# Kernel optimization log

Measured on AMD Instinct MI355X. Metric: run time of the kernel, lower is better.

Reference implementation:

```python
import jax, jax.numpy as jnp
import numpy as np

B, S, D, H, L, O = 64, 512, 512, 1024, 2, 1000


def setup_inputs() -> dict:
    key = jax.random.key(0)
    ks = jax.random.split(key, 12)
    s = 0.05
    return {
        "x": jax.random.normal(ks[0], (B, S, D), jnp.float32),
        "h0": jnp.zeros((L, B, H), jnp.float32),
        "c0": jnp.zeros((L, B, H), jnp.float32),
        "W_ih0": jax.random.normal(ks[1], (4 * H, D), jnp.float32) * s,
        "W_hh0": jax.random.normal(ks[2], (4 * H, H), jnp.float32) * s,
        "b_ih0": jax.random.normal(ks[3], (4 * H,), jnp.float32) * s,
        "b_hh0": jax.random.normal(ks[4], (4 * H,), jnp.float32) * s,
        "W_ih1": jax.random.normal(ks[5], (4 * H, H), jnp.float32) * s,
        "W_hh1": jax.random.normal(ks[6], (4 * H, H), jnp.float32) * s,
        "b_ih1": jax.random.normal(ks[7], (4 * H,), jnp.float32) * s,
        "b_hh1": jax.random.normal(ks[8], (4 * H,), jnp.float32) * s,
        "W_fc": jax.random.normal(ks[9], (O, H), jnp.float32) * s,
        "b_fc": jax.random.normal(ks[10], (O,), jnp.float32) * s,
    }


def _lstm_cell(x_t, h, c, W_ih, W_hh, b_ih, b_hh):
    # standard LSTMCell: fused 4-gate GEMM, gate order (i, f, g, o)
    gates = x_t @ W_ih.T + b_ih + h @ W_hh.T + b_hh  # [B, 4H]
    i, f, g, o = jnp.split(gates, 4, axis=-1)
    i = jax.nn.sigmoid(i)
    f = jax.nn.sigmoid(f)
    g = jnp.tanh(g)
    o = jax.nn.sigmoid(o)
    c_new = f * c + i * g
    h_new = o * jnp.tanh(c_new)
    return h_new, c_new


def reference(x, h0, c0, W_ih0, W_hh0, b_ih0, b_hh0, W_ih1, W_hh1, b_ih1, b_hh1, W_fc, b_fc):
    params = [(W_ih0, W_hh0, b_ih0, b_hh0), (W_ih1, W_hh1, b_ih1, b_hh1)]

    def step(carry, x_t):
        hs, cs = carry  # tuples of [B,H] per layer
        new_h, new_c = [], []
        inp = x_t
        for l in range(L):  # fixed small layer count
            h_l, c_l = _lstm_cell(inp, hs[l], cs[l], *params[l])
            new_h.append(h_l)
            new_c.append(c_l)
            inp = h_l
        return (tuple(new_h), tuple(new_c)), None

    xs = jnp.swapaxes(x, 0, 1)  # [S, B, D]
    init = (tuple(h0[l] for l in range(L)), tuple(c0[l] for l in range(L)))
    (hs, _), _ = jax.lax.scan(step, init, xs)
    # dropout is inference-mode identity; output_activation=None
    out = hs[-1] @ W_fc.T + b_fc  # [B, O]
    return out
```

## Files before the change

### kernel.cpp

```cpp
#include <hip/hip_runtime.h>

#define B_ 64
#define S_ 512
#define D_ 512
#define H_ 1024

typedef __attribute__((ext_vector_type(8))) short bf16x8;
typedef __attribute__((ext_vector_type(4))) float f32x4;
typedef unsigned short u16;
typedef unsigned int u32;

#define MFMA(a, b, c) __builtin_amdgcn_mfma_f32_16x16x32_bf16(a, b, c, 0, 0, 0)

__device__ __forceinline__ u16 f2bf(float f) {
    u32 u = __float_as_uint(f);
    u += 0x7fffu + ((u >> 16) & 1u);
    return (u16)(u >> 16);
}
__device__ __forceinline__ float sigm(float x) { return 1.0f / (1.0f + __expf(-x)); }
__device__ __forceinline__ float tanh_f(float x) { return 1.0f - 2.0f / (__expf(2.0f * x) + 1.0f); }

__device__ __forceinline__ bf16x8 cvt8(const float* p) {
    float4 f0 = ((const float4*)p)[0];
    float4 f1 = ((const float4*)p)[1];
    bf16x8 v;
    v[0] = (short)f2bf(f0.x); v[1] = (short)f2bf(f0.y);
    v[2] = (short)f2bf(f0.z); v[3] = (short)f2bf(f0.w);
    v[4] = (short)f2bf(f1.x); v[5] = (short)f2bf(f1.y);
    v[6] = (short)f2bf(f1.z); v[7] = (short)f2bf(f1.w);
    return v;
}

__device__ __forceinline__ void llc_ld(bf16x8& d, const u16* p) {
    asm volatile("global_load_dwordx4 %0, %1, off sc0 sc1" : "=v"(d) : "v"(p));
}
__device__ __forceinline__ void vm0() {
    asm volatile("s_waitcnt vmcnt(0)" ::: "memory");
}
__device__ __forceinline__ void fence_frag(bf16x8& d) {
    asm volatile("" : "+v"(d));
}
__device__ __forceinline__ void llc_st16(u16* p, u16 v) {
    u32 vv = v;
    asm volatile("global_store_short %0, %1, off sc0 sc1" :: "v"(p), "v"(vv) : "memory");
}

__global__ void prep_w(const float* __restrict__ Wih, const float* __restrict__ Whh,
                       u16* __restrict__ Wc, int Kx, int Kw, int total8) {
    int idx = blockIdx.x * 256 + threadIdx.x;
    if (idx >= total8) return;
    int kc8 = Kw >> 3;
    int n = idx / kc8;
    int kc = (idx - n * kc8) << 3;
    const float* src = (kc < Kx) ? (Wih + (size_t)n * Kx + kc)
                                 : (Whh + (size_t)n * (Kw - Kx) + (kc - Kx));
    *(bf16x8*)(Wc + (size_t)n * Kw + kc) = cvt8(src);
}

__global__ void prep_misc2(const float* __restrict__ h0in,
                           const float* __restrict__ bih0, const float* __restrict__ bhh0,
                           const float* __restrict__ bih1, const float* __restrict__ bhh1,
                           float* __restrict__ bias0, float* __restrict__ bias1,
                           u16* __restrict__ h0a, u16* __restrict__ h0b,
                           u16* __restrict__ h1a, u16* __restrict__ h1b,
                           int* __restrict__ bar) {
    int idx = blockIdx.x * 256 + threadIdx.x;
    if (idx < 1024) bar[idx] = 0;
    if (idx < 4096) { bias0[idx] = bih0[idx] + bhh0[idx]; return; }
    if (idx < 8192) { int i = idx - 4096; bias1[i] = bih1[i] + bhh1[i]; return; }
    int r = idx - 8192;
    if (r >= 2 * B_ * H_) return;
    int l = r >> 16;
    int rr = r & 65535;
    int b = rr >> 10, col = rr & 1023;
    int sidx = (col >> 3) * 512 + b * 8 + (col & 7);
    u16 hb = f2bf(h0in[r]);
    if (l == 0) { h0a[sidx] = hb; h0b[sidx] = hb; }
    else        { h1a[sidx] = hb; h1b[sidx] = hb; }
}

__global__ __launch_bounds__(512, 2) void lstm_persist(
    const float* __restrict__ x,
    const u16* __restrict__ W0c, const u16* __restrict__ W1c,
    const float* __restrict__ bias0, const float* __restrict__ bias1,
    const float* __restrict__ c0in,
    u16* __restrict__ h0a, u16* __restrict__ h0b,
    u16* __restrict__ h1a, u16* __restrict__ h1b,
    float* __restrict__ h1f,
    int* __restrict__ bar) {
    const int bk = blockIdx.x;
    const int cgp = bk >> 1;
    const int mh = bk & 1;
    const int tid = threadIdx.x;
    const int w = tid >> 6;
    const int lane = tid & 63;
    const int quad = lane >> 4;
    const int l16 = lane & 15;

    int gc[2];
    #pragma unroll
    for (int n = 0; n < 2; ++n) {
        int c = n * 16 + l16;
        gc[n] = (c >> 3) * 1024 + cgp * 8 + (c & 7);
    }

    bf16x8 w0x[2][2], w0h[2][4];
    bf16x8 w1f[2][8];
    #pragma unroll
    for (int n = 0; n < 2; ++n) {
        #pragma unroll
        for (int kf = 0; kf < 2; ++kf)
            w0x[n][kf] = *(const bf16x8*)(W0c + (size_t)gc[n] * 1536 + w * 64 + kf * 32 + quad * 8);
        #pragma unroll
        for (int kf = 0; kf < 4; ++kf)
            w0h[n][kf] = *(const bf16x8*)(W0c + (size_t)gc[n] * 1536 + 512 + w * 128 + kf * 32 + quad * 8);
        #pragma unroll
        for (int kf = 0; kf < 8; ++kf)
            w1f[n][kf] = *(const bf16x8*)(W1c + (size_t)gc[n] * 2048 + w * 256 + kf * 32 + quad * 8);
    }

    __shared__ float part[8 * 32 * 37];
    __shared__ float c0l[256], c1l[256];
    __shared__ float b0l[32], b1l[32];

    if (tid < 32) {
        int gg = tid >> 3, j = tid & 7;
        b0l[tid] = bias0[gg * 1024 + cgp * 8 + j];
        b1l[tid] = bias1[gg * 1024 + cgp * 8 + j];
    }
    if (tid < 256) {
        int b = tid >> 3, j = tid & 7;
        int gi = (mh * 32 + b) * 1024 + cgp * 8 + j;
        c0l[tid] = c0in[gi];
        c1l[tid] = c0in[65536 + gi];
    }
    __syncthreads();

    const int brow0 = mh * 32 + l16;
    const int brow1 = brow0 + 16;

    f32x4 xacc[2][2];
    #define XPART(t)                                                                 \
        {                                                                            \
            xacc[0][0] = (f32x4){0.f,0.f,0.f,0.f}; xacc[0][1] = (f32x4){0.f,0.f,0.f,0.f}; \
            xacc[1][0] = (f32x4){0.f,0.f,0.f,0.f}; xacc[1][1] = (f32x4){0.f,0.f,0.f,0.f}; \
            _Pragma("unroll")                                                        \
            for (int kf = 0; kf < 2; ++kf) {                                         \
                int k = w * 64 + kf * 32 + quad * 8;                                 \
                bf16x8 a0_ = cvt8(x + (size_t)brow0 * 262144 + (t) * 512 + k);       \
                bf16x8 a1_ = cvt8(x + (size_t)brow1 * 262144 + (t) * 512 + k);       \
                xacc[0][0] = MFMA(a0_, w0x[0][kf], xacc[0][0]);                      \
                xacc[0][1] = MFMA(a0_, w0x[1][kf], xacc[0][1]);                      \
                xacc[1][0] = MFMA(a1_, w0x[0][kf], xacc[1][0]);                      \
                xacc[1][1] = MFMA(a1_, w0x[1][kf], xacc[1][1]);                      \
            }                                                                        \
        }

    XPART(0);

    for (int p = 0; p <= S_; ++p) {
        const int rd = p & 1;
        const u16* h0r = rd ? h0b : h0a;
        u16*       h0w_ = rd ? h0a : h0b;
        const u16* h1r = rd ? h1b : h1a;
        u16*       h1w_ = rd ? h1a : h1b;

        if (p > 0) {
            if (tid == 0) {
                int tgt = 256 * p;
                for (int it = 0; it < 20000; ++it) {
                    if (__hip_atomic_load(&bar[0], __ATOMIC_RELAXED, __HIP_MEMORY_SCOPE_AGENT) >= tgt)
                        break;
                    __builtin_amdgcn_s_sleep(1);
                }
            }
            __syncthreads();
        }

        bf16x8 a0[4], a1[4];
        if (p < S_) {
            #pragma unroll
            for (int kf = 0; kf < 4; ++kf) {
                int k8 = w * 16 + kf * 4 + quad;
                llc_ld(a0[kf], h0r + (k8 * 64 + brow0) * 8);
                llc_ld(a1[kf], h0r + (k8 * 64 + brow1) * 8);
            }
            vm0();
            #pragma unroll
            for (int kf = 0; kf < 4; ++kf) { fence_frag(a0[kf]); fence_frag(a1[kf]); }
        }

        if (p < S_) {
            f32x4 acc00 = xacc[0][0], acc01 = xacc[0][1];
            f32x4 acc10 = xacc[1][0], acc11 = xacc[1][1];
            #pragma unroll
            for (int kf = 0; kf < 4; ++kf) {
                acc00 = MFMA(a0[kf], w0h[0][kf], acc00);
                acc01 = MFMA(a0[kf], w0h[1][kf], acc01);
                acc10 = MFMA(a1[kf], w0h[0][kf], acc10);
                acc11 = MFMA(a1[kf], w0h[1][kf], acc11);
            }
            #pragma unroll
            for (int r = 0; r < 4; ++r) {
                int r0 = quad * 4 + r, r1 = 16 + quad * 4 + r;
                part[w * 1184 + r0 * 37 + l16]      = acc00[r];
                part[w * 1184 + r0 * 37 + 16 + l16] = acc01[r];
                part[w * 1184 + r1 * 37 + l16]      = acc10[r];
                part[w * 1184 + r1 * 37 + 16 + l16] = acc11[r];
            }
        }

        if (p >= 1 && tid == 0) {
            int tgt = 256 * p;
            for (int it = 0; it < 20000; ++it) {
                if (__hip_atomic_load(&bar[32], __ATOMIC_RELAXED, __HIP_MEMORY_SCOPE_AGENT) >= tgt)
                    break;
                __builtin_amdgcn_s_sleep(1);
            }
        }
        __syncthreads();

        bf16x8 pb0[8], pb1[8];
        if (p >= 1) {
            #pragma unroll
            for (int kf = 0; kf < 8; ++kf) {
                int k = w * 256 + kf * 32;
                const u16* src = (k < 1024) ? h0r : h1r;
                int k8 = ((k & 1023) >> 3) + quad;
                llc_ld(pb0[kf], src + (k8 * 64 + brow0) * 8);
                llc_ld(pb1[kf], src + (k8 * 64 + brow1) * 8);
            }
        }

        if (p < S_ && tid < 256) {
            int b = tid >> 3, j = tid & 7;
            float g4[4];
            #pragma unroll
            for (int gg = 0; gg < 4; ++gg) {
                float s = b0l[gg * 8 + j];
                #pragma unroll
                for (int w8 = 0; w8 < 8; ++w8)
                    s += part[w8 * 1184 + b * 37 + gg * 8 + j];
                g4[gg] = s;
            }
            float c = c0l[tid];
            float cn = sigm(g4[1]) * c + sigm(g4[0]) * tanh_f(g4[2]);
            float hn = sigm(g4[3]) * tanh_f(cn);
            c0l[tid] = cn;
            llc_st16(h0w_ + cgp * 512 + (mh * 32 + b) * 8 + j, f2bf(hn));
        }
        if (p >= 1) {
            vm0();
            #pragma unroll
            for (int kf = 0; kf < 8; ++kf) { fence_frag(pb0[kf]); fence_frag(pb1[kf]); }
        }
        __syncthreads();
        if (p < S_ && tid == 0)
            __hip_atomic_fetch_add(&bar[0], 1, __ATOMIC_RELAXED, __HIP_MEMORY_SCOPE_AGENT);

        if (p >= 1) {
            f32x4 acc00 = {0.f,0.f,0.f,0.f}, acc01 = {0.f,0.f,0.f,0.f};
            f32x4 acc10 = {0.f,0.f,0.f,0.f}, acc11 = {0.f,0.f,0.f,0.f};
            #pragma unroll
            for (int kf = 0; kf < 8; ++kf) {
                acc00 = MFMA(pb0[kf], w1f[0][kf], acc00);
                acc01 = MFMA(pb0[kf], w1f[1][kf], acc01);
                acc10 = MFMA(pb1[kf], w1f[0][kf], acc10);
                acc11 = MFMA(pb1[kf], w1f[1][kf], acc11);
            }
            #pragma unroll
            for (int r = 0; r < 4; ++r) {
                int r0 = quad * 4 + r, r1 = 16 + quad * 4 + r;
                part[w * 1184 + r0 * 37 + l16]      = acc00[r];
                part[w * 1184 + r0 * 37 + 16 + l16] = acc01[r];
                part[w * 1184 + r1 * 37 + l16]      = acc10[r];
                part[w * 1184 + r1 * 37 + 16 + l16] = acc11[r];
            }
            __syncthreads();
            if (tid < 256) {
                int b = tid >> 3, j = tid & 7;
                float g4[4];
                #pragma unroll
                for (int gg = 0; gg < 4; ++gg) {
                    float s = b1l[gg * 8 + j];
                    #pragma unroll
                    for (int w8 = 0; w8 < 8; ++w8)
                        s += part[w8 * 1184 + b * 37 + gg * 8 + j];
                    g4[gg] = s;
                }
                float c = c1l[tid];
                float cn = sigm(g4[1]) * c + sigm(g4[0]) * tanh_f(g4[2]);
                float hn = sigm(g4[3]) * tanh_f(cn);
                c1l[tid] = cn;
                llc_st16(h1w_ + cgp * 512 + (mh * 32 + b) * 8 + j, f2bf(hn));
                if (p == S_) h1f[(mh * 32 + b) * 1024 + cgp * 8 + j] = hn;
            }
        }

        if (p < S_) {
            __syncthreads();
            if (tid == 0)
                __hip_atomic_fetch_add(&bar[32], 1, __ATOMIC_RELAXED, __HIP_MEMORY_SCOPE_AGENT);
            if (p + 1 < S_) XPART(p + 1);
        }
    }
}

__global__ void fc_k(const float* __restrict__ h1f, const float* __restrict__ Wfc,
                     const float* __restrict__ bfc, float* __restrict__ out) {
    int idx = blockIdx.x * 256 + threadIdx.x;
    if (idx >= 64 * 1000) return;
    int o = idx % 1000;
    int b = idx / 1000;
    const float4* hr = (const float4*)(h1f + b * H_);
    const float4* wr = (const float4*)(Wfc + (size_t)o * H_);
    float s = 0.f;
    #pragma unroll 4
    for (int k = 0; k < 256; ++k) {
        float4 a = hr[k];
        float4 w = wr[k];
        s += a.x * w.x + a.y * w.y + a.z * w.z + a.w * w.w;
    }
    out[idx] = s + bfc[o];
}

extern "C" void kernel_launch(void* const* d_in, const int* in_sizes, int n_in,
                              void* d_out, int out_size, void* d_ws, size_t ws_size,
                              hipStream_t stream) {
    const float* x    = (const float*)d_in[0];
    const float* h0in = (const float*)d_in[1];
    const float* c0in = (const float*)d_in[2];
    const float* Wih0 = (const float*)d_in[3];
    const float* Whh0 = (const float*)d_in[4];
    const float* bih0 = (const float*)d_in[5];
    const float* bhh0 = (const float*)d_in[6];
    const float* Wih1 = (const float*)d_in[7];
    const float* Whh1 = (const float*)d_in[8];
    const float* bih1 = (const float*)d_in[9];
    const float* bhh1 = (const float*)d_in[10];
    const float* Wfc  = (const float*)d_in[11];
    const float* bfc  = (const float*)d_in[12];
    float* out = (float*)d_out;

    char* ws = (char*)d_ws;
    size_t off = 0;
    auto alloc = [&](size_t bytes) {
        void* p = ws + off;
        off += (bytes + 255) & ~(size_t)255;
        return p;
    };
    u16* W0c   = (u16*)alloc((size_t)4096 * 1536 * 2);
    u16* W1c   = (u16*)alloc((size_t)4096 * 2048 * 2);
    float* bias0 = (float*)alloc(4096 * 4);
    float* bias1 = (float*)alloc(4096 * 4);
    u16* h0A   = (u16*)alloc(B_ * H_ * 2);
    u16* h0B   = (u16*)alloc(B_ * H_ * 2);
    u16* h1A   = (u16*)alloc(B_ * H_ * 2);
    u16* h1B   = (u16*)alloc(B_ * H_ * 2);
    float* h1f = (float*)alloc(B_ * H_ * 4);
    int* bar   = (int*)alloc(4096);

    prep_w<<<786432 / 256, 256, 0, stream>>>(Wih0, Whh0, W0c, 512, 1536, 786432);
    prep_w<<<1048576 / 256, 256, 0, stream>>>(Wih1, Whh1, W1c, 1024, 2048, 1048576);
    prep_misc2<<<(8192 + 2 * B_ * H_ + 255) / 256, 256, 0, stream>>>(
        h0in, bih0, bhh0, bih1, bhh1, bias0, bias1, h0A, h0B, h1A, h1B, bar);

    void* args[] = {(void*)&x, (void*)&W0c, (void*)&W1c, (void*)&bias0, (void*)&bias1,
                    (void*)&c0in, (void*)&h0A, (void*)&h0B, (void*)&h1A, (void*)&h1B,
                    (void*)&h1f, (void*)&bar};
    hipLaunchCooperativeKernel((void*)lstm_persist, dim3(256), dim3(512), args, 0, stream);

    fc_k<<<(64000 + 255) / 256, 256, 0, stream>>>(h1f, Wfc, bfc, out);
}
```

Measured before the change: 5.516 ms.

## Triple-buffer layer-0 hidden state and publish it before layer-1 work

Layer 0's hidden state now rotates through three buffers instead of two. Each block finishes the layer-0 cell update and signals the layer-0 barrier before it waits on and computes layer 1, so the next step's layer-0 work can start sooner. The wait at the top of each step now also checks the layer-1 counter from the previous step, which prevents the third buffer from being overwritten while still in use. The next step's x-projection also moves earlier to overlap the layer-1 loads, at the cost of an extra buffer, an extra block-wide sync and a longer spin limit.

```diff
diff --git a/kernel.cpp b/kernel.cpp
--- a/kernel.cpp
+++ b/kernel.cpp
@@ -61,7 +61,7 @@
                            const float* __restrict__ bih0, const float* __restrict__ bhh0,
                            const float* __restrict__ bih1, const float* __restrict__ bhh1,
                            float* __restrict__ bias0, float* __restrict__ bias1,
-                           u16* __restrict__ h0a, u16* __restrict__ h0b,
+                           u16* __restrict__ h0a, u16* __restrict__ h0b, u16* __restrict__ h0c,
                            u16* __restrict__ h1a, u16* __restrict__ h1b,
                            int* __restrict__ bar) {
     int idx = blockIdx.x * 256 + threadIdx.x;
@@ -75,7 +75,7 @@
     int b = rr >> 10, col = rr & 1023;
     int sidx = (col >> 3) * 512 + b * 8 + (col & 7);
     u16 hb = f2bf(h0in[r]);
-    if (l == 0) { h0a[sidx] = hb; h0b[sidx] = hb; }
+    if (l == 0) { h0a[sidx] = hb; h0b[sidx] = hb; h0c[sidx] = hb; }
     else        { h1a[sidx] = hb; h1b[sidx] = hb; }
 }
 
@@ -84,7 +84,7 @@
     const u16* __restrict__ W0c, const u16* __restrict__ W1c,
     const float* __restrict__ bias0, const float* __restrict__ bias1,
     const float* __restrict__ c0in,
-    u16* __restrict__ h0a, u16* __restrict__ h0b,
+    u16* __restrict__ h0a, u16* __restrict__ h0b, u16* __restrict__ h0c,
     u16* __restrict__ h1a, u16* __restrict__ h1b,
     float* __restrict__ h1f,
     int* __restrict__ bar) {
@@ -158,19 +158,23 @@
 
     XPART(0);
 
+    const u16* H0[3] = {h0a, h0b, h0c};
+    int wp = 0;
     for (int p = 0; p <= S_; ++p) {
+        const int rp = (wp == 0) ? 2 : wp - 1;
+        const u16* h0r = H0[rp];
+        u16*       h0w_ = (u16*)H0[wp];
         const int rd = p & 1;
-        const u16* h0r = rd ? h0b : h0a;
-        u16*       h0w_ = rd ? h0a : h0b;
         const u16* h1r = rd ? h1b : h1a;
         u16*       h1w_ = rd ? h1a : h1b;
 
         if (p > 0) {
             if (tid == 0) {
-                int tgt = 256 * p;
-                for (int it = 0; it < 20000; ++it) {
-                    if (__hip_atomic_load(&bar[0], __ATOMIC_RELAXED, __HIP_MEMORY_SCOPE_AGENT) >= tgt)
-                        break;
+                int tgtA = 256 * p, tgtB = 256 * (p - 1);
+                for (int it = 0; it < 40000; ++it) {
+                    int va = __hip_atomic_load(&bar[0], __ATOMIC_RELAXED, __HIP_MEMORY_SCOPE_AGENT);
+                    int vb = __hip_atomic_load(&bar[32], __ATOMIC_RELAXED, __HIP_MEMORY_SCOPE_AGENT);
+                    if (va >= tgtA && vb >= tgtB) break;
                     __builtin_amdgcn_s_sleep(1);
                 }
             }
@@ -188,9 +192,7 @@
             vm0();
             #pragma unroll
             for (int kf = 0; kf < 4; ++kf) { fence_frag(a0[kf]); fence_frag(a1[kf]); }
-        }
-
-        if (p < S_) {
+
             f32x4 acc00 = xacc[0][0], acc01 = xacc[0][1];
             f32x4 acc10 = xacc[1][0], acc11 = xacc[1][1];
             #pragma unroll
@@ -209,10 +211,31 @@
                 part[w * 1184 + r1 * 37 + 16 + l16] = acc11[r];
             }
         }
+        __syncthreads();
+        if (p < S_ && tid < 256) {
+            int b = tid >> 3, j = tid & 7;
+            float g4[4];
+            #pragma unroll
+            for (int gg = 0; gg < 4; ++gg) {
+                float s = b0l[gg * 8 + j];
+                #pragma unroll
+                for (int w8 = 0; w8 < 8; ++w8)
+                    s += part[w8 * 1184 + b * 37 + gg * 8 + j];
+                g4[gg] = s;
+            }
+            float c = c0l[tid];
+            float cn = sigm(g4[1]) * c + sigm(g4[0]) * tanh_f(g4[2]);
+            float hn = sigm(g4[3]) * tanh_f(cn);
+            c0l[tid] = cn;
+            llc_st16(h0w_ + cgp * 512 + (mh * 32 + b) * 8 + j, f2bf(hn));
+        }
+        __syncthreads();
+        if (p < S_ && tid == 0)
+            __hip_atomic_fetch_add(&bar[0], 1, __ATOMIC_RELAXED, __HIP_MEMORY_SCOPE_AGENT);
 
         if (p >= 1 && tid == 0) {
             int tgt = 256 * p;
-            for (int it = 0; it < 20000; ++it) {
+            for (int it = 0; it < 40000; ++it) {
                 if (__hip_atomic_load(&bar[32], __ATOMIC_RELAXED, __HIP_MEMORY_SCOPE_AGENT) >= tgt)
                     break;
                 __builtin_amdgcn_s_sleep(1);
@@ -231,34 +254,12 @@
                 llc_ld(pb1[kf], src + (k8 * 64 + brow1) * 8);
             }
         }
-
-        if (p < S_ && tid < 256) {
-            int b = tid >> 3, j = tid & 7;
-            float g4[4];
-            #pragma unroll
-            for (int gg = 0; gg < 4; ++gg) {
-                float s = b0l[gg * 8 + j];
-                #pragma unroll
-                for (int w8 = 0; w8 < 8; ++w8)
-                    s += part[w8 * 1184 + b * 37 + gg * 8 + j];
-                g4[gg] = s;
-            }
-            float c = c0l[tid];
-            float cn = sigm(g4[1]) * c + sigm(g4[0]) * tanh_f(g4[2]);
-            float hn = sigm(g4[3]) * tanh_f(cn);
-            c0l[tid] = cn;
-            llc_st16(h0w_ + cgp * 512 + (mh * 32 + b) * 8 + j, f2bf(hn));
-        }
+        if (p + 1 < S_) XPART(p + 1);
+
         if (p >= 1) {
             vm0();
             #pragma unroll
             for (int kf = 0; kf < 8; ++kf) { fence_frag(pb0[kf]); fence_frag(pb1[kf]); }
-        }
-        __syncthreads();
-        if (p < S_ && tid == 0)
-            __hip_atomic_fetch_add(&bar[0], 1, __ATOMIC_RELAXED, __HIP_MEMORY_SCOPE_AGENT);
-
-        if (p >= 1) {
             f32x4 acc00 = {0.f,0.f,0.f,0.f}, acc01 = {0.f,0.f,0.f,0.f};
             f32x4 acc10 = {0.f,0.f,0.f,0.f}, acc11 = {0.f,0.f,0.f,0.f};
             #pragma unroll
@@ -301,8 +302,8 @@
             __syncthreads();
             if (tid == 0)
                 __hip_atomic_fetch_add(&bar[32], 1, __ATOMIC_RELAXED, __HIP_MEMORY_SCOPE_AGENT);
-            if (p + 1 < S_) XPART(p + 1);
-        }
+        }
+        wp = (wp == 2) ? 0 : wp + 1;
     }
 }
 
@@ -355,6 +356,7 @@
     float* bias1 = (float*)alloc(4096 * 4);
     u16* h0A   = (u16*)alloc(B_ * H_ * 2);
     u16* h0B   = (u16*)alloc(B_ * H_ * 2);
+    u16* h0C   = (u16*)alloc(B_ * H_ * 2);
     u16* h1A   = (u16*)alloc(B_ * H_ * 2);
     u16* h1B   = (u16*)alloc(B_ * H_ * 2);
     float* h1f = (float*)alloc(B_ * H_ * 4);
@@ -363,11 +365,11 @@
     prep_w<<<786432 / 256, 256, 0, stream>>>(Wih0, Whh0, W0c, 512, 1536, 786432);
     prep_w<<<1048576 / 256, 256, 0, stream>>>(Wih1, Whh1, W1c, 1024, 2048, 1048576);
     prep_misc2<<<(8192 + 2 * B_ * H_ + 255) / 256, 256, 0, stream>>>(
-        h0in, bih0, bhh0, bih1, bhh1, bias0, bias1, h0A, h0B, h1A, h1B, bar);
+        h0in, bih0, bhh0, bih1, bhh1, bias0, bias1, h0A, h0B, h0C, h1A, h1B, bar);
 
     void* args[] = {(void*)&x, (void*)&W0c, (void*)&W1c, (void*)&bias0, (void*)&bias1,
-                    (void*)&c0in, (void*)&h0A, (void*)&h0B, (void*)&h1A, (void*)&h1B,
-                    (void*)&h1f, (void*)&bar};
+                    (void*)&c0in, (void*)&h0A, (void*)&h0B, (void*)&h0C,
+                    (void*)&h1A, (void*)&h1B, (void*)&h1f, (void*)&bar};
     hipLaunchCooperativeKernel((void*)lstm_persist, dim3(256), dim3(512), args, 0, stream);
 
     fc_k<<<(64000 + 255) / 256, 256, 0, stream>>>(h1f, Wfc, bfc, out);
```

New measurement: 5.855 ms. 1.06x slower.
